# Kernel tuning notes

Hardware: AMD Instinct MI355X
Metric: run time of the kernel (lower is better)

The kernel has to match this reference:

```python
import jax, jax.numpy as jnp
import numpy as np

B, R, NT = 1, 384, 4        # batch, num_res, num_templates
C_IN = 128                   # rep_2d num_c (pair channels)
C_KV = 64                    # template pair channels
H, C = 4, 64                 # num_heads, attention_num_c


def setup_inputs() -> dict:
    key = jax.random.key(0)
    ks = jax.random.split(key, 7)
    s = lambda fan_in: 1.0 / np.sqrt(fan_in)
    return {
        "z2d": jax.random.normal(ks[0], (B, R, R, C_IN), jnp.float32),
        "t2d": jax.random.normal(ks[1], (B, NT, R, R, C_KV), jnp.float32),
        # weights stored [in, out] (torch nn.Linear applies x @ W.T)
        "Wq": jax.random.normal(ks[2], (C_IN, H * C), jnp.float32) * s(C_IN),
        "Wk": jax.random.normal(ks[3], (C_KV, H * C), jnp.float32) * s(C_KV),
        "Wv": jax.random.normal(ks[4], (C_KV, H * C), jnp.float32) * s(C_KV),
        "Wo": jax.random.normal(ks[5], (H * C, C_IN), jnp.float32) * s(H * C),
        "bo": jax.random.normal(ks[6], (C_IN,), jnp.float32) * s(H * C),
    }


def reference(z2d, t2d, Wq, Wk, Wv, Wo, bo):
    b, r, _, c_in = z2d.shape
    nt = t2d.shape[1]
    P = r * r  # flattened residue-pair axis

    z = z2d.reshape(b, P, 1, c_in)                             # [b, P, 1, c_in]
    t = jnp.transpose(t2d, (0, 2, 3, 1, 4)).reshape(b, P, nt, -1)  # [b, P, K, c_kv]

    q = (z @ Wq).reshape(b, P, 1, H, C) * C ** (-0.5)          # [b, P, 1, h, c]
    k = (t @ Wk).reshape(b, P, nt, H, C)                       # [b, P, k, h, c]
    v = (t @ Wv).reshape(b, P, nt, H, C)

    logits = jnp.einsum('bpqhc,bpkhc->bphqk', q, k)            # softmax over k templates
    weights = jax.nn.softmax(logits, axis=-1)
    weighted_avg = jnp.einsum('bphqk,bpkhc->bpqhc', weights, v)  # [b, P, 1, h, c]

    out = weighted_avg.reshape(b, P, 1, H * C) @ Wo + bo
    return out.reshape(b, r, r, c_in)
```

## Files before the change

### kernel.cpp

```cpp
#include <hip/hip_runtime.h>
#include <hip/hip_bf16.h>

#define R_   384
#define P_   (R_ * R_)
#define NT_  4
#define CIN  128
#define CKV  64
#define NH   4
#define HC   256

#define TP   64
#define LDZ  136
#define LDA  280

typedef __attribute__((ext_vector_type(8))) short bf16x8;
typedef __attribute__((ext_vector_type(4))) float f32x4;
typedef __attribute__((ext_vector_type(4))) uint  u32x4;
typedef __attribute__((ext_vector_type(2))) __bf16 bfv2;

#if defined(__has_builtin)
#if __has_builtin(__builtin_amdgcn_fdot2_f32_bf16)
#define HAS_DOT2BF 1
#endif
#endif

__device__ __forceinline__ ushort f2bf_s(float f) {
    uint32_t u = __float_as_uint(f);
    u += 0x7FFFu + ((u >> 16) & 1u);
    return (ushort)(u >> 16);
}
__device__ __forceinline__ uint packbf2(float lo, float hi) {
    return (uint)f2bf_s(lo) | ((uint)f2bf_s(hi) << 16);
}
__device__ __forceinline__ uint2 pack4(const float4 v) {
    uint2 r; r.x = packbf2(v.x, v.y); r.y = packbf2(v.z, v.w); return r;
}
__device__ __forceinline__ float bflo(uint t) { return __uint_as_float(t << 16); }
__device__ __forceinline__ float bfhi(uint t) { return __uint_as_float(t & 0xffff0000u); }

__device__ __forceinline__ float dot2bf(uint a, uint b, float acc) {
#ifdef HAS_DOT2BF
    union { uint u; bfv2 v; } ua, ub;
    ua.u = a; ub.u = b;
    return __builtin_amdgcn_fdot2_f32_bf16(ua.v, ub.v, acc, false);
#else
    float r = fmaf(bflo(a), bflo(b), acc);
    return fmaf(bfhi(a), bfhi(b), r);
#endif
}

__global__ __launch_bounds__(256) void precompute_mg(
        const float* __restrict__ Wq, const float* __restrict__ Wk,
        const float* __restrict__ Wv, const float* __restrict__ Wo,
        ushort* __restrict__ Mt, ushort* __restrict__ Gt) {
    int tid = blockIdx.x * blockDim.x + threadIdx.x;
    if (tid < HC * CIN) {
        int n = tid >> 7, ci = tid & 127;
        int h = n >> 6, j = n & 63;
        float acc = 0.f;
        for (int c = 0; c < 64; ++c)
            acc += Wq[ci * HC + h * 64 + c] * Wk[j * HC + h * 64 + c];
        Mt[n * CIN + ci] = f2bf_s(acc * 0.125f);
    } else {
        int t = tid - HC * CIN;
        int co = t >> 8, n = t & 255;
        int h = n >> 6, j = n & 63;
        float acc = 0.f;
        for (int c = 0; c < 64; ++c)
            acc += Wv[j * HC + h * 64 + c] * Wo[(h * 64 + c) * CIN + co];
        Gt[co * HC + n] = f2bf_s(acc);
    }
}

__global__ __launch_bounds__(256, 2) void tpa_fused(
        const float* __restrict__ z2d, const float* __restrict__ t2d,
        const ushort* __restrict__ Mt, const ushort* __restrict__ Gt,
        const float* __restrict__ bo, float* __restrict__ out) {

    __shared__ ushort s0[TP * LDA];
    __shared__ ushort sT[TP * LDA];

    const int tid  = threadIdx.x;
    const int lane = tid & 63;
    const int wv   = tid >> 6;
    const int lr   = lane & 15;
    const int lk   = (lane >> 4) << 3;
    const int pg0  = blockIdx.x * TP;

    bf16x8 B1[4][4];
    #pragma unroll
    for (int kt = 0; kt < 4; ++kt)
        #pragma unroll
        for (int nt = 0; nt < 4; ++nt)
            B1[kt][nt] = *(const bf16x8*)(Mt + (wv * 64 + nt * 16 + lr) * CIN + kt * 32 + lk);
    bf16x8 B2[8][2];
    #pragma unroll
    for (int kt = 0; kt < 8; ++kt)
        #pragma unroll
        for (int nt = 0; nt < 2; ++nt)
            B2[kt][nt] = *(const bf16x8*)(Gt + (wv * 32 + nt * 16 + lr) * HC + kt * 32 + lk);

    const float bias0 = bo[wv * 32 + lr];
    const float bias1 = bo[wv * 32 + 16 + lr];

    #pragma unroll
    for (int i = 0; i < 8; ++i) {
        int idx = (i * 256 + tid) * 4, p = idx >> 7, c = idx & 127;
        float4 v = *(const float4*)(z2d + (size_t)(pg0 + p) * CIN + c);
        *(uint2*)&s0[p * LDZ + c] = pack4(v);
    }
    #pragma unroll
    for (int k = 0; k < NT_; ++k) {
        const float* src = t2d + ((size_t)k * P_ + pg0) * CKV;
        #pragma unroll
        for (int i = 0; i < 4; ++i) {
            int idx = (i * 256 + tid) * 4, p = idx >> 6, c = idx & 63;
            float4 v = *(const float4*)(src + p * 64 + c);
            *(uint2*)&sT[p * LDA + k * 64 + c] = pack4(v);
        }
    }
    __syncthreads();

    f32x4 acc1[4][4];
    #pragma unroll
    for (int mt = 0; mt < 4; ++mt)
        #pragma unroll
        for (int nt = 0; nt < 4; ++nt)
            acc1[mt][nt] = (f32x4){0.f, 0.f, 0.f, 0.f};
    #pragma unroll
    for (int kt = 0; kt < 4; ++kt) {
        bf16x8 af[4];
        #pragma unroll
        for (int mt = 0; mt < 4; ++mt)
            af[mt] = *(const bf16x8*)&s0[(mt * 16 + lr) * LDZ + kt * 32 + lk];
        #pragma unroll
        for (int mt = 0; mt < 4; ++mt)
            #pragma unroll
            for (int nt = 0; nt < 4; ++nt)
                acc1[mt][nt] = __builtin_amdgcn_mfma_f32_16x16x32_bf16(
                    af[mt], B1[kt][nt], acc1[mt][nt], 0, 0, 0);
    }
    __syncthreads();

    #pragma unroll
    for (int mt = 0; mt < 4; ++mt) {
        int row = mt * 16 + ((lane >> 4) << 2);
        #pragma unroll
        for (int nt = 0; nt < 4; ++nt) {
            int n = wv * 64 + nt * 16 + lr;
            #pragma unroll
            for (int r = 0; r < 4; ++r)
                s0[(row + r) * LDA + n] = f2bf_s(acc1[mt][nt][r]);
        }
    }
    asm volatile("s_waitcnt lgkmcnt(0)" ::: "memory");
    __builtin_amdgcn_sched_barrier(0);

    {
        ushort* arow = &s0[lane * LDA + wv * 64];
        const ushort* trow = &sT[lane * LDA];

        u32x4 a4[8];
        #pragma unroll
        for (int q = 0; q < 8; ++q) a4[q] = *(const u32x4*)&arow[q * 8];

        float lg[4];
        #pragma unroll
        for (int k = 0; k < 4; ++k) {
            float s = 0.f;
            #pragma unroll
            for (int q = 0; q < 8; ++q) {
                u32x4 tq = *(const u32x4*)&trow[k * 64 + q * 8];
                #pragma unroll
                for (int e = 0; e < 4; ++e)
                    s = dot2bf(a4[q][e], tq[e], s);
            }
            lg[k] = s;
        }
        float mx = fmaxf(fmaxf(lg[0], lg[1]), fmaxf(lg[2], lg[3]));
        float w0 = __expf(lg[0] - mx), w1 = __expf(lg[1] - mx);
        float w2 = __expf(lg[2] - mx), w3 = __expf(lg[3] - mx);
        float inv = 1.f / (w0 + w1 + w2 + w3);
        w0 *= inv; w1 *= inv; w2 *= inv; w3 *= inv;

        #pragma unroll
        for (int q = 0; q < 8; ++q) {
            u32x4 t0 = *(const u32x4*)&trow[q * 8];
            u32x4 t1 = *(const u32x4*)&trow[64 + q * 8];
            u32x4 t2 = *(const u32x4*)&trow[128 + q * 8];
            u32x4 t3 = *(const u32x4*)&trow[192 + q * 8];
            u32x4 o;
            #pragma unroll
            for (int e = 0; e < 4; ++e) {
                float lo = w0 * bflo(t0[e]) + w1 * bflo(t1[e]) + w2 * bflo(t2[e]) + w3 * bflo(t3[e]);
                float hi = w0 * bfhi(t0[e]) + w1 * bfhi(t1[e]) + w2 * bfhi(t2[e]) + w3 * bfhi(t3[e]);
                o[e] = packbf2(lo, hi);
            }
            *(u32x4*)&arow[q * 8] = o;
        }
    }
    __syncthreads();

    f32x4 acc2[4][2];
    #pragma unroll
    for (int mt = 0; mt < 4; ++mt)
        #pragma unroll
        for (int nt = 0; nt < 2; ++nt)
            acc2[mt][nt] = (f32x4){0.f, 0.f, 0.f, 0.f};
    #pragma unroll
    for (int kt = 0; kt < 8; ++kt) {
        bf16x8 af[4];
        #pragma unroll
        for (int mt = 0; mt < 4; ++mt)
            af[mt] = *(const bf16x8*)&s0[(mt * 16 + lr) * LDA + kt * 32 + lk];
        #pragma unroll
        for (int mt = 0; mt < 4; ++mt)
            #pragma unroll
            for (int nt = 0; nt < 2; ++nt)
                acc2[mt][nt] = __builtin_amdgcn_mfma_f32_16x16x32_bf16(
                    af[mt], B2[kt][nt], acc2[mt][nt], 0, 0, 0);
    }

    #pragma unroll
    for (int nt = 0; nt < 2; ++nt) {
        int co = wv * 32 + nt * 16 + lr;
        float bias = nt ? bias1 : bias0;
        #pragma unroll
        for (int mt = 0; mt < 4; ++mt) {
            int row = mt * 16 + ((lane >> 4) << 2);
            #pragma unroll
            for (int r = 0; r < 4; ++r)
                out[(size_t)(pg0 + row + r) * CIN + co] = acc2[mt][nt][r] + bias;
        }
    }
}

extern "C" void kernel_launch(void* const* d_in, const int* in_sizes, int n_in,
                              void* d_out, int out_size, void* d_ws, size_t ws_size,
                              hipStream_t stream) {
    const float* z2d = (const float*)d_in[0];
    const float* t2d = (const float*)d_in[1];
    const float* Wq  = (const float*)d_in[2];
    const float* Wk  = (const float*)d_in[3];
    const float* Wv  = (const float*)d_in[4];
    const float* Wo  = (const float*)d_in[5];
    const float* bo  = (const float*)d_in[6];

    ushort* Mt = (ushort*)d_ws;
    ushort* Gt = Mt + HC * CIN;

    precompute_mg<<<(2 * HC * CIN) / 256, 256, 0, stream>>>(Wq, Wk, Wv, Wo, Mt, Gt);
    tpa_fused<<<P_ / TP, 256, 0, stream>>>(z2d, t2d, Mt, Gt, bo, (float*)d_out);
}
```

Before: 82.40 us.

## Keep projected queries in MFMA registers and compute logits via shuffles, skipping LDS round-trip

```diff
diff --git a/kernel.cpp b/kernel.cpp
--- a/kernel.cpp
+++ b/kernel.cpp
@@ -1,5 +1,4 @@
 #include <hip/hip_runtime.h>
-#include <hip/hip_bf16.h>
 
 #define R_   384
 #define P_   (R_ * R_)
@@ -16,13 +15,6 @@
 typedef __attribute__((ext_vector_type(8))) short bf16x8;
 typedef __attribute__((ext_vector_type(4))) float f32x4;
 typedef __attribute__((ext_vector_type(4))) uint  u32x4;
-typedef __attribute__((ext_vector_type(2))) __bf16 bfv2;
-
-#if defined(__has_builtin)
-#if __has_builtin(__builtin_amdgcn_fdot2_f32_bf16)
-#define HAS_DOT2BF 1
-#endif
-#endif
 
 __device__ __forceinline__ ushort f2bf_s(float f) {
     uint32_t u = __float_as_uint(f);
@@ -37,17 +29,6 @@
 }
 __device__ __forceinline__ float bflo(uint t) { return __uint_as_float(t << 16); }
 __device__ __forceinline__ float bfhi(uint t) { return __uint_as_float(t & 0xffff0000u); }
-
-__device__ __forceinline__ float dot2bf(uint a, uint b, float acc) {
-#ifdef HAS_DOT2BF
-    union { uint u; bfv2 v; } ua, ub;
-    ua.u = a; ub.u = b;
-    return __builtin_amdgcn_fdot2_f32_bf16(ua.v, ub.v, acc, false);
-#else
-    float r = fmaf(bflo(a), bflo(b), acc);
-    return fmaf(bfhi(a), bfhi(b), r);
-#endif
-}
 
 __global__ __launch_bounds__(256) void precompute_mg(
         const float* __restrict__ Wq, const float* __restrict__ Wk,
@@ -60,7 +41,8 @@
         float acc = 0.f;
         for (int c = 0; c < 64; ++c)
             acc += Wq[ci * HC + h * 64 + c] * Wk[j * HC + h * 64 + c];
-        Mt[n * CIN + ci] = f2bf_s(acc * 0.125f);
+        int jp = ((j >> 2) & 3) * 16 + (j >> 4) * 4 + (j & 3);
+        Mt[(h * 64 + jp) * CIN + ci] = f2bf_s(acc * 0.125f);
     } else {
         int t = tid - HC * CIN;
         int co = t >> 8, n = t & 255;
@@ -84,7 +66,8 @@
     const int lane = tid & 63;
     const int wv   = tid >> 6;
     const int lr   = lane & 15;
-    const int lk   = (lane >> 4) << 3;
+    const int g    = lane >> 4;
+    const int g8   = g << 3;
     const int pg0  = blockIdx.x * TP;
 
     bf16x8 B1[4][4];
@@ -92,16 +75,7 @@
     for (int kt = 0; kt < 4; ++kt)
         #pragma unroll
         for (int nt = 0; nt < 4; ++nt)
-            B1[kt][nt] = *(const bf16x8*)(Mt + (wv * 64 + nt * 16 + lr) * CIN + kt * 32 + lk);
-    bf16x8 B2[8][2];
-    #pragma unroll
-    for (int kt = 0; kt < 8; ++kt)
-        #pragma unroll
-        for (int nt = 0; nt < 2; ++nt)
-            B2[kt][nt] = *(const bf16x8*)(Gt + (wv * 32 + nt * 16 + lr) * HC + kt * 32 + lk);
-
-    const float bias0 = bo[wv * 32 + lr];
-    const float bias1 = bo[wv * 32 + 16 + lr];
+            B1[kt][nt] = *(const bf16x8*)(Mt + (wv * 64 + nt * 16 + lr) * CIN + kt * 32 + g8);
 
     #pragma unroll
     for (int i = 0; i < 8; ++i) {
@@ -123,58 +97,58 @@
 
     f32x4 acc1[4][4];
     #pragma unroll
-    for (int mt = 0; mt < 4; ++mt)
+    for (int nt = 0; nt < 4; ++nt)
+        #pragma unroll
+        for (int mt = 0; mt < 4; ++mt)
+            acc1[nt][mt] = (f32x4){0.f, 0.f, 0.f, 0.f};
+    #pragma unroll
+    for (int kt = 0; kt < 4; ++kt) {
+        bf16x8 zf[4];
+        #pragma unroll
+        for (int mt = 0; mt < 4; ++mt)
+            zf[mt] = *(const bf16x8*)&s0[(mt * 16 + lr) * LDZ + kt * 32 + g8];
         #pragma unroll
         for (int nt = 0; nt < 4; ++nt)
-            acc1[mt][nt] = (f32x4){0.f, 0.f, 0.f, 0.f};
-    #pragma unroll
-    for (int kt = 0; kt < 4; ++kt) {
-        bf16x8 af[4];
-        #pragma unroll
-        for (int mt = 0; mt < 4; ++mt)
-            af[mt] = *(const bf16x8*)&s0[(mt * 16 + lr) * LDZ + kt * 32 + lk];
-        #pragma unroll
-        for (int mt = 0; mt < 4; ++mt)
+            #pragma unroll
+            for (int mt = 0; mt < 4; ++mt)
+                acc1[nt][mt] = __builtin_amdgcn_mfma_f32_16x16x32_bf16(
+                    B1[kt][nt], zf[mt], acc1[nt][mt], 0, 0, 0);
+    }
+    __syncthreads();
+
+    bf16x8 B2[8][2];
+    #pragma unroll
+    for (int kt = 0; kt < 8; ++kt)
+        #pragma unroll
+        for (int nt = 0; nt < 2; ++nt)
+            B2[kt][nt] = *(const bf16x8*)(Gt + (wv * 32 + nt * 16 + lr) * HC + kt * 32 + g8);
+    const float bias0 = bo[wv * 32 + lr];
+    const float bias1 = bo[wv * 32 + 16 + lr];
+
+    #pragma unroll
+    for (int mt = 0; mt < 4; ++mt) {
+        const int p = mt * 16 + lr;
+        u32x4 tq[NT_][2];
+        #pragma unroll
+        for (int k = 0; k < NT_; ++k) {
+            tq[k][0] = *(const u32x4*)&sT[p * LDA + k * 64 + g * 16];
+            tq[k][1] = *(const u32x4*)&sT[p * LDA + k * 64 + g * 16 + 8];
+        }
+        float lg[4];
+        #pragma unroll
+        for (int k = 0; k < NT_; ++k) {
+            float s = 0.f;
             #pragma unroll
             for (int nt = 0; nt < 4; ++nt)
-                acc1[mt][nt] = __builtin_amdgcn_mfma_f32_16x16x32_bf16(
-                    af[mt], B1[kt][nt], acc1[mt][nt], 0, 0, 0);
-    }
-    __syncthreads();
-
-    #pragma unroll
-    for (int mt = 0; mt < 4; ++mt) {
-        int row = mt * 16 + ((lane >> 4) << 2);
-        #pragma unroll
-        for (int nt = 0; nt < 4; ++nt) {
-            int n = wv * 64 + nt * 16 + lr;
-            #pragma unroll
-            for (int r = 0; r < 4; ++r)
-                s0[(row + r) * LDA + n] = f2bf_s(acc1[mt][nt][r]);
-        }
-    }
-    asm volatile("s_waitcnt lgkmcnt(0)" ::: "memory");
-    __builtin_amdgcn_sched_barrier(0);
-
-    {
-        ushort* arow = &s0[lane * LDA + wv * 64];
-        const ushort* trow = &sT[lane * LDA];
-
-        u32x4 a4[8];
-        #pragma unroll
-        for (int q = 0; q < 8; ++q) a4[q] = *(const u32x4*)&arow[q * 8];
-
-        float lg[4];
-        #pragma unroll
-        for (int k = 0; k < 4; ++k) {
-            float s = 0.f;
-            #pragma unroll
-            for (int q = 0; q < 8; ++q) {
-                u32x4 tq = *(const u32x4*)&trow[k * 64 + q * 8];
                 #pragma unroll
-                for (int e = 0; e < 4; ++e)
-                    s = dot2bf(a4[q][e], tq[e], s);
-            }
+                for (int r = 0; r < 4; ++r) {
+                    int cc = nt * 4 + r;
+                    uint tw = tq[k][cc >> 3][(cc >> 1) & 3];
+                    float tv = (cc & 1) ? bfhi(tw) : bflo(tw);
+                    s = fmaf(acc1[nt][mt][r], tv, s);
+                }
+            s += __shfl_xor(s, 16);
+            s += __shfl_xor(s, 32);
             lg[k] = s;
         }
         float mx = fmaxf(fmaxf(lg[0], lg[1]), fmaxf(lg[2], lg[3]));
@@ -184,19 +158,17 @@
         w0 *= inv; w1 *= inv; w2 *= inv; w3 *= inv;
 
         #pragma unroll
-        for (int q = 0; q < 8; ++q) {
-            u32x4 t0 = *(const u32x4*)&trow[q * 8];
-            u32x4 t1 = *(const u32x4*)&trow[64 + q * 8];
-            u32x4 t2 = *(const u32x4*)&trow[128 + q * 8];
-            u32x4 t3 = *(const u32x4*)&trow[192 + q * 8];
+        for (int j = 0; j < 2; ++j) {
             u32x4 o;
             #pragma unroll
             for (int e = 0; e < 4; ++e) {
-                float lo = w0 * bflo(t0[e]) + w1 * bflo(t1[e]) + w2 * bflo(t2[e]) + w3 * bflo(t3[e]);
-                float hi = w0 * bfhi(t0[e]) + w1 * bfhi(t1[e]) + w2 * bfhi(t2[e]) + w3 * bfhi(t3[e]);
+                uint t0 = tq[0][j][e], t1 = tq[1][j][e];
+                uint t2 = tq[2][j][e], t3 = tq[3][j][e];
+                float lo = w0 * bflo(t0) + w1 * bflo(t1) + w2 * bflo(t2) + w3 * bflo(t3);
+                float hi = w0 * bfhi(t0) + w1 * bfhi(t1) + w2 * bfhi(t2) + w3 * bfhi(t3);
                 o[e] = packbf2(lo, hi);
             }
-            *(u32x4*)&arow[q * 8] = o;
+            *(u32x4*)&s0[p * LDA + wv * 64 + g * 16 + j * 8] = o;
         }
     }
     __syncthreads();
@@ -212,7 +184,7 @@
         bf16x8 af[4];
         #pragma unroll
         for (int mt = 0; mt < 4; ++mt)
-            af[mt] = *(const bf16x8*)&s0[(mt * 16 + lr) * LDA + kt * 32 + lk];
+            af[mt] = *(const bf16x8*)&s0[(mt * 16 + lr) * LDA + kt * 32 + g8];
         #pragma unroll
         for (int mt = 0; mt < 4; ++mt)
             #pragma unroll
@@ -227,7 +199,7 @@
         float bias = nt ? bias1 : bias0;
         #pragma unroll
         for (int mt = 0; mt < 4; ++mt) {
-            int row = mt * 16 + ((lane >> 4) << 2);
+            int row = mt * 16 + g * 4;
             #pragma unroll
             for (int r = 0; r < 4; ++r)
                 out[(size_t)(pg0 + row + r) * CIN + co] = acc2[mt][nt][r] + bias;
```

Result: slower. 88.12 us (+6.9%).
